# Kernel tuning notes

Hardware: AMD Instinct MI355X
Metric: run time of the kernel (lower is better)

The kernel has to match this reference:

```python
import jax, jax.numpy as jnp
import numpy as np

INPUT_DIM = 1024
OUTPUT_DIM = 1024
DEGREE = 8
N_TOKENS = 8192


def setup_inputs() -> dict:
    key = jax.random.key(0)
    k1, k2 = jax.random.split(key)
    x = jax.random.normal(k1, (N_TOKENS, INPUT_DIM), dtype=jnp.float32)
    # xavier_normal_ with gain = 1/(input_dim*(degree+1)) over fan dims (output_dim, degree+1)
    fan_in, fan_out = OUTPUT_DIM, DEGREE + 1  # torch treats dim0/dim1 as fans; scale is tiny anyway
    gain = 1.0 / (INPUT_DIM * (DEGREE + 1))
    std = gain * np.sqrt(2.0 / (INPUT_DIM + OUTPUT_DIM))
    cheby_coeffs = std * jax.random.normal(k2, (INPUT_DIM, OUTPUT_DIM, DEGREE + 1), dtype=jnp.float32)
    return {"x": x, "cheby_coeffs": cheby_coeffs}


def reference(x, cheby_coeffs):
    # x: (..., input_dim) -> y: (..., output_dim)
    degree_p1 = cheby_coeffs.shape[-1]
    theta = jnp.arccos(jnp.tanh(x))                      # (..., i)
    arange = jnp.arange(degree_p1, dtype=x.dtype)        # (d,)
    basis = jnp.cos(theta[..., None] * arange)           # (..., i, d) Chebyshev T_d(tanh(x))
    y = jnp.einsum('...id,iod->...o', basis, cheby_coeffs)
    return y
```

## Files before the change

kernel.cpp:

```cpp
#include <hip/hip_runtime.h>


typedef __bf16 bf16;
typedef __bf16 bf16x8 __attribute__((ext_vector_type(8)));
typedef float f32x2 __attribute__((ext_vector_type(2)));
typedef float f32x4 __attribute__((ext_vector_type(4)));
typedef float f32x16 __attribute__((ext_vector_type(16)));

__device__ __forceinline__ void g2lds16(const void* g, void* l) {
  __builtin_amdgcn_global_load_lds(
      (const __attribute__((address_space(1))) unsigned int*)g,
      (__attribute__((address_space(3))) unsigned int*)l, 16, 0, 0);
}

__device__ __forceinline__ float fast_tanh(float a) {
  float e = __expf(a + a);
  return 1.f - 2.f * __builtin_amdgcn_rcpf(e + 1.f);
}

__global__ __launch_bounds__(256)
void cheby_prep(const float* __restrict__ x, const float* __restrict__ C,
                bf16* __restrict__ Bt, float* __restrict__ bias_p,
                float* __restrict__ th) {
  const int bid = blockIdx.x, tid = threadIdx.x;
  if (bid >= 1024) {
    const int r = bid - 1024;
    f32x4 v = *(const f32x4*)(x + (size_t)r * 1024 + tid * 4);
    f32x4 t;
    #pragma unroll
    for (int j = 0; j < 4; ++j) t[j] = fast_tanh(v[j]);
    *(f32x2*)(th + (size_t)r * 1024 + tid * 2)       = (f32x2){t.x, t.z};
    *(f32x2*)(th + (size_t)r * 1024 + 512 + tid * 2) = (f32x2){t.y, t.w};
    return;
  }
  __shared__ float tile[32][292];
  const int i0 = (bid >> 5) * 32, o0 = (bid & 31) * 32;
  {
    const int r = tid >> 3, seg = tid & 7;
    const float* src = C + (size_t)(i0 + r) * 9216 + (size_t)o0 * 9 + seg * 36;
    float* dst = &tile[r][seg * 36];
    #pragma unroll
    for (int v = 0; v < 9; ++v) *(f32x4*)(dst + v * 4) = *(const f32x4*)(src + v * 4);
  }
  __syncthreads();
  #pragma unroll
  for (int j = 0; j < 4; ++j) {
    int e = tid + 256 * j;
    int il = e >> 5, ol = e & 31;
    int i = i0 + il, o = o0 + ol;
    bf16x8 v;
    #pragma unroll
    for (int d = 0; d < 8; ++d) v[d] = (bf16)tile[il][ol * 9 + 1 + d];
    size_t idx16 = ((size_t)((o >> 7) * 128 + (i >> 3)) * 8 + (i & 7)) * 128 + (o & 127);
    *(bf16x8*)&Bt[idx16 * 8] = v;
  }
  if (tid < 32) {
    float s = 0.f;
    #pragma unroll
    for (int i = 0; i < 32; ++i) s += tile[i][tid * 9];
    bias_p[(size_t)(bid >> 5) * 1024 + o0 + tid] = s;
  }
}

__global__ __launch_bounds__(256, 2)
void cheby_gemm(const float* __restrict__ th, const bf16* __restrict__ Bt,
                const float* __restrict__ bias_p, float* __restrict__ out) {
  __shared__ bf16 Bs[2][8192];

  const int tid  = threadIdx.x;
  const int lane = tid & 63, w = tid >> 6;
  const int wm = w >> 1, wn = w & 1;
  const int nb = blockIdx.x & 7, mb = blockIdx.x >> 3;
  const int t0 = mb * 128, o0 = nb * 128;
  const int ml = lane & 31, h = lane >> 5;

  const float* xr0 = th + (size_t)(t0 + wm * 64 + ml) * 1024 + h * 512;
  const float* xr1 = xr0 + 32 * 1024;
  const bf16* btw = Bt + ((size_t)nb * 128 * 1024 + (size_t)w * 256 + lane) * 8;

  f32x16 acc[2][2];
  #pragma unroll
  for (int a = 0; a < 2; ++a)
    #pragma unroll
    for (int b = 0; b < 2; ++b)
      #pragma unroll
      for (int r = 0; r < 16; ++r) acc[a][b][r] = 0.f;

  bf16x8 afrA[2][4], afrB[2][4];
  f32x4 xv0, xv1;

  auto gen = [&](bf16x8 (&dst)[2][4], f32x4 s0, f32x4 s1) {
    #pragma unroll
    for (int ks = 0; ks < 4; ++ks) {
      f32x2 t  = {s0[ks], s1[ks]};
      f32x2 t2 = t + t;
      f32x2 prev = {1.f, 1.f}, cur = t;
      #pragma unroll
      for (int j = 0; j < 8; ++j) {
        dst[0][ks][j] = (bf16)cur.x;
        dst[1][ks][j] = (bf16)cur.y;
        f32x2 nx = t2 * cur - prev;
        prev = cur; cur = nx;
      }
    }
  };

  {
    f32x4 s0 = *(const f32x4*)(xr0), s1 = *(const f32x4*)(xr1);
    gen(afrA, s0, s1);
    xv0 = *(const f32x4*)(xr0 + 4);
    xv1 = *(const f32x4*)(xr1 + 4);
  }
  #pragma unroll
  for (int b = 0; b < 4; ++b)
    g2lds16(btw + (size_t)b * 64 * 8, &Bs[0][(w * 256 + b * 64) * 8]);

  auto stage = [&](int s, int bi, bf16x8 (&cur)[2][4], bf16x8 (&nxt)[2][4]) {
    __syncthreads();
    if (s < 127) {
      const bf16* g = btw + (size_t)(s + 1) * 8192;
      #pragma unroll
      for (int b = 0; b < 4; ++b)
        g2lds16(g + (size_t)b * 64 * 8, &Bs[bi ^ 1][(w * 256 + b * 64) * 8]);
    }
    bf16x8 bfr[4][2];
    #pragma unroll
    for (int ks = 0; ks < 4; ++ks) {
      const int ce = ((ks * 2 + h) * 128 + wn * 64 + ml) * 8;
      bfr[ks][0] = *(const bf16x8*)&Bs[bi][ce];
      bfr[ks][1] = *(const bf16x8*)&Bs[bi][ce + 32 * 8];
    }
    if (s < 127) {
      gen(nxt, xv0, xv1);
      if (s < 126) {
        xv0 = *(const f32x4*)(xr0 + (s + 2) * 4);
        xv1 = *(const f32x4*)(xr1 + (s + 2) * 4);
      }
    }
    #pragma unroll
    for (int ks = 0; ks < 4; ++ks) {
      acc[0][0] = __builtin_amdgcn_mfma_f32_32x32x16_bf16(cur[0][ks], bfr[ks][0], acc[0][0], 0, 0, 0);
      acc[0][1] = __builtin_amdgcn_mfma_f32_32x32x16_bf16(cur[0][ks], bfr[ks][1], acc[0][1], 0, 0, 0);
      acc[1][0] = __builtin_amdgcn_mfma_f32_32x32x16_bf16(cur[1][ks], bfr[ks][0], acc[1][0], 0, 0, 0);
      acc[1][1] = __builtin_amdgcn_mfma_f32_32x32x16_bf16(cur[1][ks], bfr[ks][1], acc[1][1], 0, 0, 0);
    }
  };

  #pragma unroll 1
  for (int s2 = 0; s2 < 64; ++s2) {
    stage(2 * s2,     0, afrA, afrB);
    stage(2 * s2 + 1, 1, afrB, afrA);
  }

  const int c0 = o0 + wn * 64 + ml;
  float bv0 = 0.f, bv1 = 0.f;
  #pragma unroll
  for (int p = 0; p < 32; ++p) {
    bv0 += bias_p[(size_t)p * 1024 + c0];
    bv1 += bias_p[(size_t)p * 1024 + c0 + 32];
  }
  #pragma unroll
  for (int mt = 0; mt < 2; ++mt)
    #pragma unroll
    for (int r = 0; r < 16; ++r) {
      int row = t0 + wm * 64 + mt * 32 + (r & 3) + 8 * (r >> 2) + 4 * h;
      float* po = out + (size_t)row * 1024 + c0;
      po[0]  = acc[mt][0][r] + bv0;
      po[32] = acc[mt][1][r] + bv1;
    }
}

__global__ __launch_bounds__(256)
void cheby_naive(const float* __restrict__ x, const float* __restrict__ C,
                 float* __restrict__ out) {
  const int t = blockIdx.x, tid = threadIdx.x;
  float acc[4] = {0.f, 0.f, 0.f, 0.f};
  for (int i = 0; i < 1024; ++i) {
    float th = tanhf(x[(size_t)t * 1024 + i]);
    float T[9]; T[0] = 1.f; T[1] = th;
    #pragma unroll
    for (int d = 2; d < 9; ++d) T[d] = 2.f * th * T[d - 1] - T[d - 2];
    #pragma unroll
    for (int j = 0; j < 4; ++j) {
      const float* cp = &C[((size_t)i * 1024 + tid + j * 256) * 9];
      float s = 0.f;
      #pragma unroll
      for (int d = 0; d < 9; ++d) s += T[d] * cp[d];
      acc[j] += s;
    }
  }
  #pragma unroll
  for (int j = 0; j < 4; ++j) out[(size_t)t * 1024 + tid + j * 256] = acc[j];
}

extern "C" void kernel_launch(void* const* d_in, const int* in_sizes, int n_in,
                              void* d_out, int out_size, void* d_ws, size_t ws_size,
                              hipStream_t stream) {
  (void)in_sizes; (void)n_in; (void)out_size;
  const float* x = (const float*)d_in[0];
  const float* C = (const float*)d_in[1];
  float* out = (float*)d_out;

  const size_t bt_bytes = (size_t)8 * 128 * 1024 * 8 * sizeof(bf16);
  const size_t bp_bytes = (size_t)32 * 1024 * sizeof(float);
  const size_t th_bytes = (size_t)8192 * 1024 * sizeof(float);

  if (ws_size >= bt_bytes + bp_bytes + th_bytes) {
    bf16*  Bt     = (bf16*)d_ws;
    float* bias_p = (float*)((char*)d_ws + bt_bytes);
    float* th     = (float*)((char*)d_ws + bt_bytes + bp_bytes);
    cheby_prep<<<9216, 256, 0, stream>>>(x, C, Bt, bias_p, th);
    cheby_gemm<<<512, 256, 0, stream>>>(th, Bt, bias_p, out);
  } else {
    cheby_naive<<<8192, 256, 0, stream>>>(x, C, out);
  }
}
```

Baseline: 272.4 us.

## Materialize bf16 Chebyshev basis in prep kernel and stream it via LDS

A new prep kernel computes tanh and the full Chebyshev basis for every token and stores it as a pre-swizzled bf16 A matrix (128 MB), alongside B in an MFMA-friendly layout. The new GEMM then does no basis generation: it streams A into LDS with direct global-to-LDS loads, loads B fragments straight into registers with lookahead, and uses explicit waitcnt, barriers and setprio around the MFMA groups. It also remaps block indices so that neighbouring blocks share N tiles. This removes the in-loop recurrence ALU work from the GEMM, at the cost of writing and reading a large extra intermediate through HBM, and it depends on the workspace being large enough.

```diff
diff --git a/kernel.cpp b/kernel.cpp
--- a/kernel.cpp
+++ b/kernel.cpp
@@ -7,6 +7,8 @@
 typedef float f32x4 __attribute__((ext_vector_type(4)));
 typedef float f32x16 __attribute__((ext_vector_type(16)));
 
+#define MFMA __builtin_amdgcn_mfma_f32_32x32x16_bf16
+
 __device__ __forceinline__ void g2lds16(const void* g, void* l) {
   __builtin_amdgcn_global_load_lds(
       (const __attribute__((address_space(1))) unsigned int*)g,
@@ -16,6 +18,191 @@
 __device__ __forceinline__ float fast_tanh(float a) {
   float e = __expf(a + a);
   return 1.f - 2.f * __builtin_amdgcn_rcpf(e + 1.f);
+}
+
+
+__global__ __launch_bounds__(256)
+void cheby_prep2(const float* __restrict__ x, const float* __restrict__ C,
+                 bf16* __restrict__ A, bf16* __restrict__ B,
+                 float* __restrict__ bias_p) {
+  const int bid = blockIdx.x, tid = threadIdx.x;
+  if (bid < 512) {
+    const int mb = bid >> 3, ig = bid & 7;
+    const int rl = tid & 127, ih = tid >> 7;
+    const int m32 = rl >> 5, ml = rl & 31;
+    const int i_base = ig * 128 + ih * 64;
+    const float* xp = x + (size_t)(mb * 128 + rl) * 1024 + i_base;
+    bf16* aout = A + (size_t)mb * 128 * 8192;
+    #pragma unroll 2
+    for (int q = 0; q < 16; ++q) {
+      f32x4 xv = *(const f32x4*)(xp + q * 4);
+      #pragma unroll
+      for (int j = 0; j < 4; ++j) {
+        const int ia = i_base + q * 4 + j;
+        const int kt = ia >> 3, cc = ia & 7;
+        float z = fast_tanh(xv[j]);
+        float z2 = z + z, pv = 1.f, cv = z;
+        bf16x8 v;
+        #pragma unroll
+        for (int d = 0; d < 8; ++d) {
+          v[d] = (bf16)cv;
+          float nx = z2 * cv - pv; pv = cv; cv = nx;
+        }
+        const int widx = (((cc >> 1) * 4 + m32) * 2 + (cc & 1)) * 32 + ml;
+        *(bf16x8*)(aout + (size_t)kt * 8192 + widx * 8) = v;
+      }
+    }
+    return;
+  }
+  const int b2 = bid - 512;
+  __shared__ float tile[32][292];
+  const int i0 = (b2 >> 5) * 32, o0 = (b2 & 31) * 32;
+  {
+    const int r = tid >> 3, seg = tid & 7;
+    const float* src = C + (size_t)(i0 + r) * 9216 + (size_t)o0 * 9 + seg * 36;
+    float* dst = &tile[r][seg * 36];
+    #pragma unroll
+    for (int v = 0; v < 9; ++v) *(f32x4*)(dst + v * 4) = *(const f32x4*)(src + v * 4);
+  }
+  __syncthreads();
+  #pragma unroll
+  for (int j = 0; j < 4; ++j) {
+    int e = tid + 256 * j;
+    int il = e >> 5, ol = e & 31;
+    int i = i0 + il, o = o0 + ol;
+    bf16x8 v;
+    #pragma unroll
+    for (int d = 0; d < 8; ++d) v[d] = (bf16)tile[il][ol * 9 + 1 + d];
+    const int cc = i & 7;
+    size_t tnum = (size_t)(o >> 7) * 128 + (i >> 3);
+    const int widx = (((cc >> 1) * 4 + ((o & 127) >> 5)) * 2 + (cc & 1)) * 32 + (o & 31);
+    *(bf16x8*)(B + tnum * 8192 + widx * 8) = v;
+  }
+  if (tid < 32) {
+    float s = 0.f;
+    #pragma unroll
+    for (int i = 0; i < 32; ++i) s += tile[i][tid * 9];
+    bias_p[(size_t)(b2 >> 5) * 1024 + o0 + tid] = s;
+  }
+}
+
+__global__ __launch_bounds__(256, 2)
+void cheby_gemm2(const bf16* __restrict__ A, const bf16* __restrict__ B,
+                 const float* __restrict__ bias_p, float* __restrict__ out) {
+  __shared__ bf16 As[2][8192];
+  const int tid = threadIdx.x;
+  const int lane = tid & 63, w = tid >> 6;
+  const int wm = w >> 1, wn = w & 1;
+  const int bid = blockIdx.x;
+  const int mb = (bid & 7) * 8 + ((bid >> 3) & 7);
+  const int nb = bid >> 6;
+
+  const bf16* aG = A + (size_t)mb * 128 * 8192 + (w * 4) * 512 + lane * 8;
+  const bf16* bG = B + (size_t)nb * 128 * 8192 + wn * 1024 + lane * 8;
+
+  f32x16 acc[2][2];
+  #pragma unroll
+  for (int a = 0; a < 2; ++a)
+    #pragma unroll
+    for (int b = 0; b < 2; ++b)
+      #pragma unroll
+      for (int r = 0; r < 16; ++r) acc[a][b][r] = 0.f;
+
+  bf16x8 bA[4][2], bB[4][2];
+
+  auto issueA = [&](int t, int p) {
+    const bf16* g = aG + (size_t)t * 8192;
+    #pragma unroll
+    for (int c = 0; c < 4; ++c)
+      g2lds16(g + c * 512, &As[p][(w * 4 + c) * 512]);
+  };
+  auto loadB = [&](bf16x8 (&dst)[4][2], int t) {
+    const bf16* g = bG + (size_t)t * 8192;
+    #pragma unroll
+    for (int ks = 0; ks < 4; ++ks)
+      #pragma unroll
+      for (int nt = 0; nt < 2; ++nt)
+        dst[ks][nt] = *(const bf16x8*)(g + (ks * 256 + nt * 64) * 8);
+  };
+
+  issueA(0, 0);
+  loadB(bA, 0);
+  loadB(bB, 1);
+
+  auto tilestep = [&](int t, int p, bf16x8 (&cur)[4][2]) {
+    const bf16* aL = &As[p][(wm * 128 + lane) * 8];
+    if (t + 1 < 128) {
+      issueA(t + 1, p ^ 1);
+      asm volatile("s_waitcnt vmcnt(12)" ::: "memory");
+    } else {
+      asm volatile("s_waitcnt vmcnt(0)" ::: "memory");
+    }
+    __builtin_amdgcn_s_barrier();
+    asm volatile("" ::: "memory");
+    {
+      bf16x8 a00 = *(const bf16x8*)(aL);
+      bf16x8 a01 = *(const bf16x8*)(aL + 64 * 8);
+      bf16x8 a10 = *(const bf16x8*)(aL + 256 * 8);
+      bf16x8 a11 = *(const bf16x8*)(aL + 320 * 8);
+      __builtin_amdgcn_s_setprio(1);
+      acc[0][0] = MFMA(a00, cur[0][0], acc[0][0], 0, 0, 0);
+      acc[0][1] = MFMA(a00, cur[0][1], acc[0][1], 0, 0, 0);
+      acc[1][0] = MFMA(a01, cur[0][0], acc[1][0], 0, 0, 0);
+      acc[1][1] = MFMA(a01, cur[0][1], acc[1][1], 0, 0, 0);
+      acc[0][0] = MFMA(a10, cur[1][0], acc[0][0], 0, 0, 0);
+      acc[0][1] = MFMA(a10, cur[1][1], acc[0][1], 0, 0, 0);
+      acc[1][0] = MFMA(a11, cur[1][0], acc[1][0], 0, 0, 0);
+      acc[1][1] = MFMA(a11, cur[1][1], acc[1][1], 0, 0, 0);
+      __builtin_amdgcn_s_setprio(0);
+    }
+    asm volatile("" ::: "memory");
+    __builtin_amdgcn_s_barrier();
+    asm volatile("" ::: "memory");
+    {
+      bf16x8 a20 = *(const bf16x8*)(aL + 512 * 8);
+      bf16x8 a21 = *(const bf16x8*)(aL + 576 * 8);
+      bf16x8 a30 = *(const bf16x8*)(aL + 768 * 8);
+      bf16x8 a31 = *(const bf16x8*)(aL + 832 * 8);
+      __builtin_amdgcn_s_setprio(1);
+      acc[0][0] = MFMA(a20, cur[2][0], acc[0][0], 0, 0, 0);
+      acc[0][1] = MFMA(a20, cur[2][1], acc[0][1], 0, 0, 0);
+      acc[1][0] = MFMA(a21, cur[2][0], acc[1][0], 0, 0, 0);
+      acc[1][1] = MFMA(a21, cur[2][1], acc[1][1], 0, 0, 0);
+      acc[0][0] = MFMA(a30, cur[3][0], acc[0][0], 0, 0, 0);
+      acc[0][1] = MFMA(a30, cur[3][1], acc[0][1], 0, 0, 0);
+      acc[1][0] = MFMA(a31, cur[3][0], acc[1][0], 0, 0, 0);
+      acc[1][1] = MFMA(a31, cur[3][1], acc[1][1], 0, 0, 0);
+      __builtin_amdgcn_s_setprio(0);
+    }
+    if (t + 2 < 128) loadB(cur, t + 2);
+    asm volatile("" ::: "memory");
+    __builtin_amdgcn_s_barrier();
+    asm volatile("" ::: "memory");
+  };
+
+  #pragma unroll 1
+  for (int t2 = 0; t2 < 128; t2 += 2) {
+    tilestep(t2, 0, bA);
+    tilestep(t2 + 1, 1, bB);
+  }
+
+  const int h = lane >> 5, ml = lane & 31;
+  const int c0 = nb * 128 + wn * 64 + ml;
+  float bv0 = 0.f, bv1 = 0.f;
+  #pragma unroll
+  for (int p = 0; p < 32; ++p) {
+    bv0 += bias_p[(size_t)p * 1024 + c0];
+    bv1 += bias_p[(size_t)p * 1024 + c0 + 32];
+  }
+  #pragma unroll
+  for (int mt = 0; mt < 2; ++mt)
+    #pragma unroll
+    for (int r = 0; r < 16; ++r) {
+      int row = mb * 128 + wm * 64 + mt * 32 + (r & 3) + 8 * (r >> 2) + 4 * h;
+      float* po = out + (size_t)row * 1024 + c0;
+      po[0]  = acc[mt][0][r] + bv0;
+      po[32] = acc[mt][1][r] + bv1;
+    }
 }
 
 __global__ __launch_bounds__(256)
@@ -66,7 +253,6 @@
 void cheby_gemm(const float* __restrict__ th, const bf16* __restrict__ Bt,
                 const float* __restrict__ bias_p, float* __restrict__ out) {
   __shared__ bf16 Bs[2][8192];
-
   const int tid  = threadIdx.x;
   const int lane = tid & 63, w = tid >> 6;
   const int wm = w >> 1, wn = w & 1;
@@ -139,10 +325,10 @@
     }
     #pragma unroll
     for (int ks = 0; ks < 4; ++ks) {
-      acc[0][0] = __builtin_amdgcn_mfma_f32_32x32x16_bf16(cur[0][ks], bfr[ks][0], acc[0][0], 0, 0, 0);
-      acc[0][1] = __builtin_amdgcn_mfma_f32_32x32x16_bf16(cur[0][ks], bfr[ks][1], acc[0][1], 0, 0, 0);
-      acc[1][0] = __builtin_amdgcn_mfma_f32_32x32x16_bf16(cur[1][ks], bfr[ks][0], acc[1][0], 0, 0, 0);
-      acc[1][1] = __builtin_amdgcn_mfma_f32_32x32x16_bf16(cur[1][ks], bfr[ks][1], acc[1][1], 0, 0, 0);
+      acc[0][0] = MFMA(cur[0][ks], bfr[ks][0], acc[0][0], 0, 0, 0);
+      acc[0][1] = MFMA(cur[0][ks], bfr[ks][1], acc[0][1], 0, 0, 0);
+      acc[1][0] = MFMA(cur[1][ks], bfr[ks][0], acc[1][0], 0, 0, 0);
+      acc[1][1] = MFMA(cur[1][ks], bfr[ks][1], acc[1][1], 0, 0, 0);
     }
   };
 
@@ -201,11 +387,20 @@
   const float* C = (const float*)d_in[1];
   float* out = (float*)d_out;
 
-  const size_t bt_bytes = (size_t)8 * 128 * 1024 * 8 * sizeof(bf16);
-  const size_t bp_bytes = (size_t)32 * 1024 * sizeof(float);
-  const size_t th_bytes = (size_t)8192 * 1024 * sizeof(float);
-
-  if (ws_size >= bt_bytes + bp_bytes + th_bytes) {
+  const size_t a_bytes  = (size_t)8192 * 8192 * 2;
+  const size_t b_bytes  = (size_t)8 * 128 * 8192 * 2;
+  const size_t bp_bytes = (size_t)32 * 1024 * 4;
+
+  const size_t bt_bytes = (size_t)8 * 128 * 1024 * 8 * 2;
+  const size_t th_bytes = (size_t)8192 * 1024 * 4;
+
+  if (ws_size >= a_bytes + b_bytes + bp_bytes) {
+    bf16*  A      = (bf16*)d_ws;
+    bf16*  B      = (bf16*)((char*)d_ws + a_bytes);
+    float* bias_p = (float*)((char*)d_ws + a_bytes + b_bytes);
+    cheby_prep2<<<1536, 256, 0, stream>>>(x, C, A, B, bias_p);
+    cheby_gemm2<<<512, 256, 0, stream>>>(A, B, bias_p, out);
+  } else if (ws_size >= bt_bytes + bp_bytes + th_bytes) {
     bf16*  Bt     = (bf16*)d_ws;
     float* bias_p = (float*)((char*)d_ws + bt_bytes);
     float* th     = (float*)((char*)d_ws + bt_bytes + bp_bytes);
```

Result: slower. 286.4 us (+5.1%).

## Precompute bf16 Chebyshev basis in prep, stream both operands via LDS ring

Applied to the files above, without the earlier changes.

The prep kernel now evaluates tanh and the Chebyshev recurrence once and writes the full bf16 basis matrix A (8192x8192) in an MFMA-fragment-friendly tiled layout, so the GEMM no longer regenerates the basis from fp32 inputs per tile. The GEMM becomes a 512-thread, 256x128-tile kernel that streams both A and B through a 3-stage LDS ring with global_load_lds, explicit vmcnt waits, split barriers and setprio around MFMA bursts. Block IDs are remapped so neighbouring blocks share B tiles. The cost is a 128 MB intermediate write and read of A, and a ring that uses most of LDS with one block per CU.

```diff
diff --git a/kernel.cpp b/kernel.cpp
--- a/kernel.cpp
+++ b/kernel.cpp
@@ -7,6 +7,8 @@
 typedef float f32x4 __attribute__((ext_vector_type(4)));
 typedef float f32x16 __attribute__((ext_vector_type(16)));
 
+#define MFMA __builtin_amdgcn_mfma_f32_32x32x16_bf16
+
 __device__ __forceinline__ void g2lds16(const void* g, void* l) {
   __builtin_amdgcn_global_load_lds(
       (const __attribute__((address_space(1))) unsigned int*)g,
@@ -19,22 +21,43 @@
 }
 
 __global__ __launch_bounds__(256)
-void cheby_prep(const float* __restrict__ x, const float* __restrict__ C,
-                bf16* __restrict__ Bt, float* __restrict__ bias_p,
-                float* __restrict__ th) {
+void cheby_prep3(const float* __restrict__ x, const float* __restrict__ C,
+                 bf16* __restrict__ A, bf16* __restrict__ B,
+                 float* __restrict__ bias_p) {
   const int bid = blockIdx.x, tid = threadIdx.x;
-  if (bid >= 1024) {
-    const int r = bid - 1024;
-    f32x4 v = *(const f32x4*)(x + (size_t)r * 1024 + tid * 4);
-    f32x4 t;
-    #pragma unroll
-    for (int j = 0; j < 4; ++j) t[j] = fast_tanh(v[j]);
-    *(f32x2*)(th + (size_t)r * 1024 + tid * 2)       = (f32x2){t.x, t.z};
-    *(f32x2*)(th + (size_t)r * 1024 + 512 + tid * 2) = (f32x2){t.y, t.w};
+  if (bid < 2048) {
+    const int rb = bid >> 4, ig = bid & 15;
+    const int rl = tid & 63, ih = tid >> 6;
+    const int i_base = ig * 64 + ih * 16;
+    const int mb = rb >> 1;
+    const int rs = (rb & 1) * 64 + rl;
+    const int m32 = rs >> 5, ml = rs & 31;
+    const float* xp = x + (size_t)(rb * 64 + rl) * 1024 + i_base;
+    bf16* aout = A + (size_t)mb * 1048576;
+    #pragma unroll
+    for (int q = 0; q < 4; ++q) {
+      f32x4 xv = *(const f32x4*)(xp + q * 4);
+      #pragma unroll
+      for (int j = 0; j < 4; ++j) {
+        const int ia = i_base + q * 4 + j;
+        const int kt = ia >> 3, cc = ia & 7;
+        float z = fast_tanh(xv[j]);
+        float z2 = z + z, pv = 1.f, cv = z;
+        bf16x8 v;
+        #pragma unroll
+        for (int d = 0; d < 8; ++d) {
+          v[d] = (bf16)cv;
+          float nx = z2 * cv - pv; pv = cv; cv = nx;
+        }
+        const int widx = (((cc >> 1) * 4 + m32) * 2 + (cc & 1)) * 32 + ml;
+        *(bf16x8*)(aout + (size_t)kt * 8192 + widx * 8) = v;
+      }
+    }
     return;
   }
+  const int b2 = bid - 2048;
   __shared__ float tile[32][292];
-  const int i0 = (bid >> 5) * 32, o0 = (bid & 31) * 32;
+  const int i0 = (b2 >> 5) * 32, o0 = (b2 & 31) * 32;
   {
     const int r = tid >> 3, seg = tid & 7;
     const float* src = C + (size_t)(i0 + r) * 9216 + (size_t)o0 * 9 + seg * 36;
@@ -51,32 +74,39 @@
     bf16x8 v;
     #pragma unroll
     for (int d = 0; d < 8; ++d) v[d] = (bf16)tile[il][ol * 9 + 1 + d];
-    size_t idx16 = ((size_t)((o >> 7) * 128 + (i >> 3)) * 8 + (i & 7)) * 128 + (o & 127);
-    *(bf16x8*)&Bt[idx16 * 8] = v;
+    const int cc = i & 7;
+    size_t tnum = (size_t)(o >> 7) * 128 + (i >> 3);
+    const int widx = (((cc >> 1) * 4 + ((o & 127) >> 5)) * 2 + (cc & 1)) * 32 + (o & 31);
+    *(bf16x8*)(B + tnum * 8192 + widx * 8) = v;
   }
   if (tid < 32) {
     float s = 0.f;
     #pragma unroll
     for (int i = 0; i < 32; ++i) s += tile[i][tid * 9];
-    bias_p[(size_t)(bid >> 5) * 1024 + o0 + tid] = s;
-  }
-}
-
-__global__ __launch_bounds__(256, 2)
-void cheby_gemm(const float* __restrict__ th, const bf16* __restrict__ Bt,
-                const float* __restrict__ bias_p, float* __restrict__ out) {
-  __shared__ bf16 Bs[2][8192];
-
-  const int tid  = threadIdx.x;
+    bias_p[(size_t)(b2 >> 5) * 1024 + o0 + tid] = s;
+  }
+}
+
+__global__ __launch_bounds__(512, 1)
+void cheby_gemm4(const bf16* __restrict__ A, const bf16* __restrict__ B,
+                 const float* __restrict__ bias_p, float* __restrict__ out) {
+  __shared__ bf16 ring[3][24576];
+  const int tid = threadIdx.x;
   const int lane = tid & 63, w = tid >> 6;
   const int wm = w >> 1, wn = w & 1;
-  const int nb = blockIdx.x & 7, mb = blockIdx.x >> 3;
-  const int t0 = mb * 128, o0 = nb * 128;
+  const int bid = blockIdx.x;
+  const int wgid = (bid & 7) * 32 + (bid >> 3);
+  const int mb2 = wgid >> 3, nb = wgid & 7;
+
   const int ml = lane & 31, h = lane >> 5;
-
-  const float* xr0 = th + (size_t)(t0 + wm * 64 + ml) * 1024 + h * 512;
-  const float* xr1 = xr0 + 32 * 1024;
-  const bf16* btw = Bt + ((size_t)nb * 128 * 1024 + (size_t)w * 256 + lane) * 8;
+  const int aLane = h * 256 + ml * 8;
+  const int row0 = wm * 64, row1 = row0 + 32;
+  const int aBase0 = (row0 >> 7) * 8192 + ((row0 >> 5) & 3) * 512 + aLane;
+  const int aBase1 = (row1 >> 7) * 8192 + ((row1 >> 5) & 3) * 512 + aLane;
+  const int bBase  = 16384 + wn * 1024 + aLane;
+
+  const bf16* aG = A + (size_t)(mb2 * 2) * 1048576 + tid * 8;
+  const bf16* bG = B + (size_t)nb * 1048576 + tid * 8;
 
   f32x16 acc[2][2];
   #pragma unroll
@@ -86,84 +116,97 @@
       #pragma unroll
       for (int r = 0; r < 16; ++r) acc[a][b][r] = 0.f;
 
-  bf16x8 afrA[2][4], afrB[2][4];
-  f32x4 xv0, xv1;
-
-  auto gen = [&](bf16x8 (&dst)[2][4], f32x4 s0, f32x4 s1) {
-    #pragma unroll
-    for (int ks = 0; ks < 4; ++ks) {
-      f32x2 t  = {s0[ks], s1[ks]};
-      f32x2 t2 = t + t;
-      f32x2 prev = {1.f, 1.f}, cur = t;
-      #pragma unroll
-      for (int j = 0; j < 8; ++j) {
-        dst[0][ks][j] = (bf16)cur.x;
-        dst[1][ks][j] = (bf16)cur.y;
-        f32x2 nx = t2 * cur - prev;
-        prev = cur; cur = nx;
-      }
-    }
+  auto issueA01 = [&](int t, int p) {
+    g2lds16(aG + (size_t)t * 8192,        &ring[p][tid * 8]);
+    g2lds16(aG + (size_t)t * 8192 + 4096, &ring[p][4096 + tid * 8]);
   };
-
-  {
-    f32x4 s0 = *(const f32x4*)(xr0), s1 = *(const f32x4*)(xr1);
-    gen(afrA, s0, s1);
-    xv0 = *(const f32x4*)(xr0 + 4);
-    xv1 = *(const f32x4*)(xr1 + 4);
-  }
-  #pragma unroll
-  for (int b = 0; b < 4; ++b)
-    g2lds16(btw + (size_t)b * 64 * 8, &Bs[0][(w * 256 + b * 64) * 8]);
-
-  auto stage = [&](int s, int bi, bf16x8 (&cur)[2][4], bf16x8 (&nxt)[2][4]) {
-    __syncthreads();
-    if (s < 127) {
-      const bf16* g = btw + (size_t)(s + 1) * 8192;
-      #pragma unroll
-      for (int b = 0; b < 4; ++b)
-        g2lds16(g + (size_t)b * 64 * 8, &Bs[bi ^ 1][(w * 256 + b * 64) * 8]);
-    }
-    bf16x8 bfr[4][2];
-    #pragma unroll
-    for (int ks = 0; ks < 4; ++ks) {
-      const int ce = ((ks * 2 + h) * 128 + wn * 64 + ml) * 8;
-      bfr[ks][0] = *(const bf16x8*)&Bs[bi][ce];
-      bfr[ks][1] = *(const bf16x8*)&Bs[bi][ce + 32 * 8];
-    }
-    if (s < 127) {
-      gen(nxt, xv0, xv1);
-      if (s < 126) {
-        xv0 = *(const f32x4*)(xr0 + (s + 2) * 4);
-        xv1 = *(const f32x4*)(xr1 + (s + 2) * 4);
-      }
-    }
-    #pragma unroll
-    for (int ks = 0; ks < 4; ++ks) {
-      acc[0][0] = __builtin_amdgcn_mfma_f32_32x32x16_bf16(cur[0][ks], bfr[ks][0], acc[0][0], 0, 0, 0);
-      acc[0][1] = __builtin_amdgcn_mfma_f32_32x32x16_bf16(cur[0][ks], bfr[ks][1], acc[0][1], 0, 0, 0);
-      acc[1][0] = __builtin_amdgcn_mfma_f32_32x32x16_bf16(cur[1][ks], bfr[ks][0], acc[1][0], 0, 0, 0);
-      acc[1][1] = __builtin_amdgcn_mfma_f32_32x32x16_bf16(cur[1][ks], bfr[ks][1], acc[1][1], 0, 0, 0);
-    }
+  auto issueA23B = [&](int t, int p) {
+    g2lds16(aG + 1048576 + (size_t)t * 8192,        &ring[p][8192 + tid * 8]);
+    g2lds16(aG + 1048576 + (size_t)t * 8192 + 4096, &ring[p][12288 + tid * 8]);
+    g2lds16(bG + (size_t)t * 8192,                  &ring[p][16384 + tid * 8]);
+    g2lds16(bG + (size_t)t * 8192 + 4096,           &ring[p][20480 + tid * 8]);
   };
 
+  issueA01(0, 0); issueA23B(0, 0);
+  issueA01(1, 1); issueA23B(1, 1);
+  asm volatile("s_waitcnt vmcnt(6)" ::: "memory");
+  __builtin_amdgcn_s_barrier();
+
+  auto step = [&](int t, int pc, int pn) {
+    const bf16* ra = &ring[pc][0];
+    const bool pf = (t + 2 < 128);
+    {
+      bf16x8 a00 = *(const bf16x8*)(ra + aBase0);
+      bf16x8 a10 = *(const bf16x8*)(ra + aBase1);
+      bf16x8 a01 = *(const bf16x8*)(ra + aBase0 + 2048);
+      bf16x8 a11 = *(const bf16x8*)(ra + aBase1 + 2048);
+      bf16x8 b00 = *(const bf16x8*)(ra + bBase);
+      bf16x8 b10 = *(const bf16x8*)(ra + bBase + 512);
+      bf16x8 b01 = *(const bf16x8*)(ra + bBase + 2048);
+      bf16x8 b11 = *(const bf16x8*)(ra + bBase + 2048 + 512);
+      if (pf) issueA01(t + 2, pn);
+      __builtin_amdgcn_s_barrier();
+      __builtin_amdgcn_s_setprio(1);
+      acc[0][0] = MFMA(a00, b00, acc[0][0], 0, 0, 0);
+      acc[0][1] = MFMA(a00, b10, acc[0][1], 0, 0, 0);
+      acc[1][0] = MFMA(a10, b00, acc[1][0], 0, 0, 0);
+      acc[1][1] = MFMA(a10, b10, acc[1][1], 0, 0, 0);
+      acc[0][0] = MFMA(a01, b01, acc[0][0], 0, 0, 0);
+      acc[0][1] = MFMA(a01, b11, acc[0][1], 0, 0, 0);
+      acc[1][0] = MFMA(a11, b01, acc[1][0], 0, 0, 0);
+      acc[1][1] = MFMA(a11, b11, acc[1][1], 0, 0, 0);
+      __builtin_amdgcn_s_setprio(0);
+      __builtin_amdgcn_s_barrier();
+    }
+    {
+      bf16x8 a02 = *(const bf16x8*)(ra + aBase0 + 4096);
+      bf16x8 a12 = *(const bf16x8*)(ra + aBase1 + 4096);
+      bf16x8 a03 = *(const bf16x8*)(ra + aBase0 + 4096 + 2048);
+      bf16x8 a13 = *(const bf16x8*)(ra + aBase1 + 4096 + 2048);
+      bf16x8 b02 = *(const bf16x8*)(ra + bBase + 4096);
+      bf16x8 b12 = *(const bf16x8*)(ra + bBase + 4096 + 512);
+      bf16x8 b03 = *(const bf16x8*)(ra + bBase + 4096 + 2048);
+      bf16x8 b13 = *(const bf16x8*)(ra + bBase + 4096 + 2048 + 512);
+      if (pf) issueA23B(t + 2, pn);
+      if (t < 126) asm volatile("s_waitcnt vmcnt(6)" ::: "memory");
+      else         asm volatile("s_waitcnt vmcnt(0)" ::: "memory");
+      __builtin_amdgcn_s_barrier();
+      __builtin_amdgcn_s_setprio(1);
+      acc[0][0] = MFMA(a02, b02, acc[0][0], 0, 0, 0);
+      acc[0][1] = MFMA(a02, b12, acc[0][1], 0, 0, 0);
+      acc[1][0] = MFMA(a12, b02, acc[1][0], 0, 0, 0);
+      acc[1][1] = MFMA(a12, b12, acc[1][1], 0, 0, 0);
+      acc[0][0] = MFMA(a03, b03, acc[0][0], 0, 0, 0);
+      acc[0][1] = MFMA(a03, b13, acc[0][1], 0, 0, 0);
+      acc[1][0] = MFMA(a13, b03, acc[1][0], 0, 0, 0);
+      acc[1][1] = MFMA(a13, b13, acc[1][1], 0, 0, 0);
+      __builtin_amdgcn_s_setprio(0);
+      __builtin_amdgcn_s_barrier();
+    }
+  };
+
   #pragma unroll 1
-  for (int s2 = 0; s2 < 64; ++s2) {
-    stage(2 * s2,     0, afrA, afrB);
-    stage(2 * s2 + 1, 1, afrB, afrA);
-  }
-
-  const int c0 = o0 + wn * 64 + ml;
+  for (int t3 = 0; t3 < 126; t3 += 3) {
+    step(t3,     0, 2);
+    step(t3 + 1, 1, 0);
+    step(t3 + 2, 2, 1);
+  }
+  step(126, 0, 2);
+  step(127, 1, 0);
+
+  const int c0 = nb * 128 + wn * 64 + ml;
   float bv0 = 0.f, bv1 = 0.f;
   #pragma unroll
   for (int p = 0; p < 32; ++p) {
     bv0 += bias_p[(size_t)p * 1024 + c0];
     bv1 += bias_p[(size_t)p * 1024 + c0 + 32];
   }
+  const int r0 = mb2 * 256 + wm * 64;
   #pragma unroll
   for (int mt = 0; mt < 2; ++mt)
     #pragma unroll
     for (int r = 0; r < 16; ++r) {
-      int row = t0 + wm * 64 + mt * 32 + (r & 3) + 8 * (r >> 2) + 4 * h;
+      int row = r0 + mt * 32 + (r & 3) + 8 * (r >> 2) + 4 * h;
       float* po = out + (size_t)row * 1024 + c0;
       po[0]  = acc[mt][0][r] + bv0;
       po[32] = acc[mt][1][r] + bv1;
@@ -201,16 +244,16 @@
   const float* C = (const float*)d_in[1];
   float* out = (float*)d_out;
 
-  const size_t bt_bytes = (size_t)8 * 128 * 1024 * 8 * sizeof(bf16);
-  const size_t bp_bytes = (size_t)32 * 1024 * sizeof(float);
-  const size_t th_bytes = (size_t)8192 * 1024 * sizeof(float);
-
-  if (ws_size >= bt_bytes + bp_bytes + th_bytes) {
-    bf16*  Bt     = (bf16*)d_ws;
-    float* bias_p = (float*)((char*)d_ws + bt_bytes);
-    float* th     = (float*)((char*)d_ws + bt_bytes + bp_bytes);
-    cheby_prep<<<9216, 256, 0, stream>>>(x, C, Bt, bias_p, th);
-    cheby_gemm<<<512, 256, 0, stream>>>(th, Bt, bias_p, out);
+  const size_t a_bytes  = (size_t)8192 * 8192 * 2;
+  const size_t b_bytes  = (size_t)8 * 128 * 8192 * 2;
+  const size_t bp_bytes = (size_t)32 * 1024 * 4;
+
+  if (ws_size >= a_bytes + b_bytes + bp_bytes) {
+    bf16*  A      = (bf16*)d_ws;
+    bf16*  B      = (bf16*)((char*)d_ws + a_bytes);
+    float* bias_p = (float*)((char*)d_ws + a_bytes + b_bytes);
+    cheby_prep3<<<3072, 256, 0, stream>>>(x, C, A, B, bias_p);
+    cheby_gemm4<<<256, 512, 0, stream>>>(A, B, bias_p, out);
   } else {
     cheby_naive<<<8192, 256, 0, stream>>>(x, C, out);
   }
```

After: 254.4 us. 6.6% less time.
